# Optimization experiments

Hardware: AMD Instinct MI355X
Metric: run time of the kernel (lower is better)

Reference implementation:

```python
import jax, jax.numpy as jnp
import numpy as np

NUM_STAB = 1e-3  # numerical_stabilizer for relu kernel


def _relu_feature(x, proj):
    # x: [B, L, H, D], proj: [M, D] -> [B, L, H, M]
    ratio = 1.0 / jnp.sqrt(jnp.asarray(proj.shape[0], x.dtype))
    return jax.nn.relu(ratio * jnp.einsum('blhd,md->blhm', x, proj)) + NUM_STAB


def setup_inputs() -> dict:
    key = jax.random.key(0)
    k1, k2, k3, k4, k5 = jax.random.split(key, 5)
    B, L, H, D, M = 16, 576, 12, 64, 8  # L = length_of_side**2 = 24**2
    return {
        'query': jax.random.normal(k1, (B, L, H, D), dtype=jnp.float32),
        'key': jax.random.normal(k2, (B, L, H, D), dtype=jnp.float32),
        'value': jax.random.normal(k3, (B, L, H, D), dtype=jnp.float32),
        'projection_matrix': jax.random.normal(k4, (M, D), dtype=jnp.float32),
        # RPE mask is nonnegative per-head mixing matrix [H, L, L]
        'mask_matrix': jax.random.uniform(k5, (H, L, L), dtype=jnp.float32),
    }


def reference(query, key, value, projection_matrix, mask_matrix):
    # ReLU kernel features (projection_matrix_type='relu')
    q_prime = _relu_feature(query, projection_matrix)  # [B, L, H, M]
    k_prime = _relu_feature(key, projection_matrix)    # [B, L, H, M]
    B, L, H, M = k_prime.shape
    D = value.shape[-1]

    # D_1[b,l,h,m,d] = k'[b,l,h,m] * v[b,l,h,d], flattened over (m,d)
    D_1 = jnp.einsum('blhm,blhd->blhmd', k_prime, value).reshape(B, L, H, M * D)
    # mask-matrix causal/RPE mixing over the L dimension (per head)
    D_1_hat = jnp.einsum('hij,bjhc->bihc', mask_matrix, D_1).reshape(B, L, H, M, D)
    D_2_hat = jnp.einsum('hij,bjhm->bihm', mask_matrix, k_prime)  # [B, L, H, M]

    av_attention = jnp.einsum('blhm,blhmd->blhd', q_prime, D_1_hat)  # [B, L, H, D]
    ks_sum = jnp.sum(D_2_hat, axis=1)                                # [B, H, M]
    normalizer = jnp.einsum('blhm,bhm->blh', q_prime, ks_sum)        # [B, L, H]
    return av_attention / normalizer[..., None]
```

## Files before the change

### kernel.cpp

```cpp
#include <hip/hip_runtime.h>


#define B_ 16
#define L_ 576
#define H_ 12
#define D_ 64
#define M_ 8
#define NUM_STAB 1e-3f
#define RATIO 0.35355339059327373f

typedef __attribute__((ext_vector_type(8))) short short8;
typedef __attribute__((ext_vector_type(4))) float f32x4;

union Pack {
    uint4 u4;
    short8 s8;
    uint2 u2[2];
    unsigned u[4];
    unsigned short us[8];
};

__device__ inline unsigned short f2bf(float x) {
    union { float f; unsigned u; } a; a.f = x;
    unsigned r = (a.u + 0x7FFFu + ((a.u >> 16) & 1u)) >> 16;
    return (unsigned short)r;
}

#define WS_QP_OFF (H_ * L_)
#define QP_ELEMS  ((size_t)B_ * H_ * L_ * M_)

__global__ __launch_bounds__(256) void feat_kernel(const float* __restrict__ q,
                                                   const float* __restrict__ k,
                                                   const float* __restrict__ proj,
                                                   const float* __restrict__ mask,
                                                   unsigned short* __restrict__ qp,
                                                   unsigned short* __restrict__ kp,
                                                   float* __restrict__ cmask) {
    __shared__ float cred[4][16];
    const int lc = blockIdx.x, h = blockIdx.y, b = blockIdx.z, t = threadIdx.x;
    const int wv = t >> 6, l = t & 63, r8 = l >> 3, c8 = l & 7;
    const int row = lc * 32 + wv * 8 + r8;

    float4 pj0[8], pj1[8];
#pragma unroll
    for (int m = 0; m < 8; ++m) {
        pj0[m] = *(const float4*)(proj + m * 64 + c8 * 8);
        pj1[m] = *(const float4*)(proj + m * 64 + c8 * 8 + 4);
    }

#pragma unroll
    for (int s = 0; s < 2; ++s) {
        const float* src = s ? k : q;
        unsigned short* dst = s ? kp : qp;
        const float* xp = src + (((size_t)b * L_ + row) * H_ + h) * D_ + c8 * 8;
        float4 x0 = *(const float4*)xp;
        float4 x1 = *(const float4*)(xp + 4);
        x0.x *= RATIO; x0.y *= RATIO; x0.z *= RATIO; x0.w *= RATIO;
        x1.x *= RATIO; x1.y *= RATIO; x1.z *= RATIO; x1.w *= RATIO;
        float p[8];
#pragma unroll
        for (int m = 0; m < 8; ++m) {
            p[m] = x0.x * pj0[m].x + x0.y * pj0[m].y + x0.z * pj0[m].z + x0.w * pj0[m].w
                 + x1.x * pj1[m].x + x1.y * pj1[m].y + x1.z * pj1[m].z + x1.w * pj1[m].w;
        }
#pragma unroll
        for (int st = 1; st <= 4; st <<= 1) {
#pragma unroll
            for (int m = 0; m < 8; ++m) p[m] += __shfl_xor(p[m], st, 64);
        }
        float r = p[0];
        r = (c8 == 1) ? p[1] : r;
        r = (c8 == 2) ? p[2] : r;
        r = (c8 == 3) ? p[3] : r;
        r = (c8 == 4) ? p[4] : r;
        r = (c8 == 5) ? p[5] : r;
        r = (c8 == 6) ? p[6] : r;
        r = (c8 == 7) ? p[7] : r;
        r = fmaxf(r, 0.f) + NUM_STAB;
        dst[((size_t)(b * H_ + h) * L_ + row) * 8 + c8] = f2bf(r);
    }

    if (b < 2) {
        const int c = t & 15, rg = t >> 4;
        const int col0 = lc * 32 + b * 16;
        const float* mb = mask + (size_t)h * L_ * L_ + col0 + c;
        float a = 0.f;
#pragma unroll 4
        for (int k2 = 0; k2 < 36; ++k2) a += mb[(size_t)(rg + 16 * k2) * L_];
        a += __shfl_xor(a, 16, 64);
        a += __shfl_xor(a, 32, 64);
        if ((l >> 4) == 0) cred[wv][c] = a;
        __syncthreads();
        if (t < 16) cmask[h * L_ + col0 + t] = cred[0][t] + cred[1][t] + cred[2][t] + cred[3][t];
    }
}

__global__ __launch_bounds__(256, 4) void attn_kernel(const float* __restrict__ v,
                                                      const float* __restrict__ mask,
                                                      const unsigned short* __restrict__ qp,
                                                      const unsigned short* __restrict__ kp,
                                                      const float* __restrict__ cmask,
                                                      float* __restrict__ out) {
    __shared__ __align__(16) unsigned short Sp[4 * 16 * 40];
    __shared__ __align__(16) unsigned short Bt[2][64 * 40];
    __shared__ float cm_s[L_];

    const int t = threadIdx.x;
    int id = blockIdx.x;
    const int bhi = id & 7; id >>= 3;
    const int blo = id & 1; id >>= 1;
    const int it = id % 9, h = id / 9;
    const int b = bhi * 2 + blo;
    const int i0 = it * 64;

    const int wv = t >> 6, l = t & 63, c15 = l & 15, kq = l >> 4;

    cm_s[t] = cmask[h * L_ + t];
    cm_s[t + 256] = cmask[h * L_ + t + 256];
    if (t < 64) cm_s[t + 512] = cmask[h * L_ + t + 512];

    const float* maskbase = mask + (size_t)h * L_ * L_ + (size_t)(i0 + 16 * wv + c15) * L_;
    const unsigned short* kpb = kp + (size_t)(b * H_ + h) * L_ * 8;
    const float* vb = v + ((size_t)b * L_ * H_ + h) * D_ + l;

    short8 Bq;
    {
        Pack pk; pk.u4 = make_uint4(0, 0, 0, 0);
        if (kq == 0) {
            const unsigned short* qpb = qp + ((size_t)(b * H_ + h) * L_ + i0 + 16 * wv + c15) * 8;
            pk.u4 = *(const uint4*)qpb;
        }
        Bq = pk.s8;
    }

    unsigned short* SpW = Sp + wv * 16 * 40;

    f32x4 acc0 = {0.f, 0.f, 0.f, 0.f}, acc1 = acc0, acc2 = acc0, acc3 = acc0;
    float nacc = 0.f;

    float vf[8];
    float4 mv0, mv1;
    uint4 kraw = make_uint4(0, 0, 0, 0);
    {
#pragma unroll
        for (int qv = 0; qv < 8; ++qv) vf[qv] = vb[(size_t)(8 * wv + qv) * (H_ * D_)];
        mv0 = *(const float4*)(maskbase + 4 * kq);
        mv1 = *(const float4*)(maskbase + 16 + 4 * kq);
        if (kq < 2) kraw = *(const uint4*)(kpb + (size_t)(16 * kq + c15) * 8);
    }

    __syncthreads();

    for (int jt = 0; jt < 18; ++jt) {
        const int j0 = jt * 32;
        const int slab = jt & 1;

        Pack a0, a1;
        a1.u[0] = __shfl_down(kraw.x, 16, 64);
        a1.u[1] = __shfl_down(kraw.y, 16, 64);
        a1.u[2] = __shfl_down(kraw.z, 16, 64);
        a1.u[3] = __shfl_down(kraw.w, 16, 64);
        if (kq == 0) {
            a0.u4 = kraw;
        } else {
            a0.u4 = make_uint4(0, 0, 0, 0);
            a1.u4 = make_uint4(0, 0, 0, 0);
        }
        const f32x4 zz = {0.f, 0.f, 0.f, 0.f};
        f32x4 s0 = __builtin_amdgcn_mfma_f32_16x16x32_bf16(a0.s8, Bq, zz, 0, 0, 0);
        f32x4 s1 = __builtin_amdgcn_mfma_f32_16x16x32_bf16(a1.s8, Bq, zz, 0, 0, 0);

        {
            Pack pv;
#pragma unroll
            for (int qv = 0; qv < 8; ++qv) pv.us[qv] = f2bf(vf[qv]);
            *(uint4*)&Bt[slab][l * 40 + 8 * wv] = pv.u4;
        }
        {
            float4 cm0 = *(const float4*)&cm_s[j0 + 4 * kq];
            float4 cm1 = *(const float4*)&cm_s[j0 + 16 + 4 * kq];
            nacc += cm0.x * s0[0] + cm0.y * s0[1] + cm0.z * s0[2] + cm0.w * s0[3]
                  + cm1.x * s1[0] + cm1.y * s1[1] + cm1.z * s1[2] + cm1.w * s1[3];
            Pack ps;
            ps.us[0] = f2bf(s0[0] * mv0.x);
            ps.us[1] = f2bf(s0[1] * mv0.y);
            ps.us[2] = f2bf(s0[2] * mv0.z);
            ps.us[3] = f2bf(s0[3] * mv0.w);
            ps.us[4] = f2bf(s1[0] * mv1.x);
            ps.us[5] = f2bf(s1[1] * mv1.y);
            ps.us[6] = f2bf(s1[2] * mv1.z);
            ps.us[7] = f2bf(s1[3] * mv1.w);
            *(uint2*)&SpW[c15 * 40 + 4 * kq] = ps.u2[0];
            *(uint2*)&SpW[c15 * 40 + 16 + 4 * kq] = ps.u2[1];
        }
        {
            const int jn = (jt < 17) ? j0 + 32 : 0;
#pragma unroll
            for (int qv = 0; qv < 8; ++qv) vf[qv] = vb[(size_t)(jn + 8 * wv + qv) * (H_ * D_)];
            mv0 = *(const float4*)(maskbase + jn + 4 * kq);
            mv1 = *(const float4*)(maskbase + jn + 16 + 4 * kq);
            if (kq < 2) kraw = *(const uint4*)(kpb + (size_t)(jn + 16 * kq + c15) * 8);
        }
        __syncthreads();

        {
            short8 As = *(const short8*)&SpW[c15 * 40 + kq * 8];
            short8 B0 = *(const short8*)&Bt[slab][c15 * 40 + kq * 8];
            short8 B1 = *(const short8*)&Bt[slab][(16 + c15) * 40 + kq * 8];
            short8 B2 = *(const short8*)&Bt[slab][(32 + c15) * 40 + kq * 8];
            short8 B3 = *(const short8*)&Bt[slab][(48 + c15) * 40 + kq * 8];
            acc0 = __builtin_amdgcn_mfma_f32_16x16x32_bf16(As, B0, acc0, 0, 0, 0);
            acc1 = __builtin_amdgcn_mfma_f32_16x16x32_bf16(As, B1, acc1, 0, 0, 0);
            acc2 = __builtin_amdgcn_mfma_f32_16x16x32_bf16(As, B2, acc2, 0, 0, 0);
            acc3 = __builtin_amdgcn_mfma_f32_16x16x32_bf16(As, B3, acc3, 0, 0, 0);
        }
    }

    nacc += __shfl_xor(nacc, 16, 64);
    nacc += __shfl_xor(nacc, 32, 64);
    float iv[4];
#pragma unroll
    for (int r = 0; r < 4; ++r) iv[r] = 1.0f / __shfl(nacc, 4 * kq + r, 64);

    float* ob = out + (((size_t)b * L_ + i0 + 16 * wv + 4 * kq) * H_ + h) * D_ + c15;
    const f32x4 aa[4] = {acc0, acc1, acc2, acc3};
#pragma unroll
    for (int di = 0; di < 4; ++di)
#pragma unroll
        for (int r = 0; r < 4; ++r)
            ob[(size_t)r * (H_ * D_) + 16 * di] = aa[di][r] * iv[r];
}

extern "C" void kernel_launch(void* const* d_in, const int* in_sizes, int n_in,
                              void* d_out, int out_size, void* d_ws, size_t ws_size,
                              hipStream_t stream) {
    const float* q    = (const float*)d_in[0];
    const float* k    = (const float*)d_in[1];
    const float* v    = (const float*)d_in[2];
    const float* proj = (const float*)d_in[3];
    const float* mask = (const float*)d_in[4];
    float* out = (float*)d_out;

    float* ws = (float*)d_ws;
    float* cmask = ws;
    unsigned short* qp_w = (unsigned short*)(ws + WS_QP_OFF);
    unsigned short* kp_w = qp_w + QP_ELEMS;

    feat_kernel<<<dim3(L_ / 32, H_, B_), 256, 0, stream>>>(q, k, proj, mask, qp_w, kp_w, cmask);
    attn_kernel<<<1728, 256, 0, stream>>>(v, mask, qp_w, kp_w, cmask, out);
}
```

Measured before the change: 182.8 us.

## Double the j-tile to 64 per iteration and use packed bf16 conversion

The attention kernel now processes 64 key positions per loop iteration instead of 32. This halves the iteration count and the number of block barriers, and each iteration gets more MFMA work and larger batches of loads. The column-mask sums are permuted in shared memory so each lane reads them as scalar loads, and float-to-bf16 rounding uses the packed HIP intrinsic instead of manual bit rounding. The cost is more registers for v, mask and k prefetch and larger LDS tiles, which may reduce occupancy at the four-blocks-per-CU launch bound.

```diff
diff --git a/kernel.cpp b/kernel.cpp
--- a/kernel.cpp
+++ b/kernel.cpp
@@ -1,4 +1,5 @@
 #include <hip/hip_runtime.h>
+#include <hip/hip_bf16.h>
 
 
 #define B_ 16
@@ -24,6 +25,11 @@
     union { float f; unsigned u; } a; a.f = x;
     unsigned r = (a.u + 0x7FFFu + ((a.u >> 16) & 1u)) >> 16;
     return (unsigned short)r;
+}
+__device__ inline unsigned pk2(float lo, float hi) {
+    __hip_bfloat162 h = __float22bfloat162_rn(make_float2(lo, hi));
+    union { __hip_bfloat162 b; unsigned u; } c; c.b = h;
+    return c.u;
 }
 
 #define WS_QP_OFF (H_ * L_)
@@ -101,9 +107,9 @@
                                                       const unsigned short* __restrict__ kp,
                                                       const float* __restrict__ cmask,
                                                       float* __restrict__ out) {
-    __shared__ __align__(16) unsigned short Sp[4 * 16 * 40];
-    __shared__ __align__(16) unsigned short Bt[2][64 * 40];
-    __shared__ float cm_s[L_];
+    __shared__ __align__(16) unsigned short Sp[4 * 16 * 72];
+    __shared__ __align__(16) unsigned short Bt[2][64 * 72];
+    __shared__ float cms[576];
 
     const int t = threadIdx.x;
     int id = blockIdx.x;
@@ -115,9 +121,19 @@
 
     const int wv = t >> 6, l = t & 63, c15 = l & 15, kq = l >> 4;
 
-    cm_s[t] = cmask[h * L_ + t];
-    cm_s[t + 256] = cmask[h * L_ + t + 256];
-    if (t < 64) cm_s[t + 512] = cmask[h * L_ + t + 512];
+    {
+        const float* cmg = cmask + h * L_;
+#pragma unroll
+        for (int rep = 0; rep < 3; ++rep) {
+            int idx = t + rep * 256;
+            if (idx < 576) {
+                int p = idx / 36, rem = idx - p * 36;
+                int jt9 = rem >> 2, kqi = rem & 3;
+                int j = jt9 * 64 + ((p >> 2) << 4) + 4 * kqi + (p & 3);
+                cms[idx] = cmg[j];
+            }
+        }
+    }
 
     const float* maskbase = mask + (size_t)h * L_ * L_ + (size_t)(i0 + 16 * wv + c15) * L_;
     const unsigned short* kpb = kp + (size_t)(b * H_ + h) * L_ * 8;
@@ -133,86 +149,99 @@
         Bq = pk.s8;
     }
 
-    unsigned short* SpW = Sp + wv * 16 * 40;
+    unsigned short* SpW = Sp + wv * 16 * 72;
 
     f32x4 acc0 = {0.f, 0.f, 0.f, 0.f}, acc1 = acc0, acc2 = acc0, acc3 = acc0;
     float nacc = 0.f;
 
-    float vf[8];
-    float4 mv0, mv1;
-    uint4 kraw = make_uint4(0, 0, 0, 0);
+    float vf[16];
+    float4 mv[4];
+    uint4 kraw0 = make_uint4(0, 0, 0, 0), kraw1 = kraw0;
     {
 #pragma unroll
-        for (int qv = 0; qv < 8; ++qv) vf[qv] = vb[(size_t)(8 * wv + qv) * (H_ * D_)];
-        mv0 = *(const float4*)(maskbase + 4 * kq);
-        mv1 = *(const float4*)(maskbase + 16 + 4 * kq);
-        if (kq < 2) kraw = *(const uint4*)(kpb + (size_t)(16 * kq + c15) * 8);
+        for (int qv = 0; qv < 16; ++qv) vf[qv] = vb[(size_t)(16 * wv + qv) * (H_ * D_)];
+#pragma unroll
+        for (int T = 0; T < 4; ++T) mv[T] = *(const float4*)(maskbase + 16 * T + 4 * kq);
+        if (kq < 2) {
+            kraw0 = *(const uint4*)(kpb + (size_t)(16 * kq + c15) * 8);
+            kraw1 = *(const uint4*)(kpb + (size_t)(32 + 16 * kq + c15) * 8);
+        }
     }
 
     __syncthreads();
 
-    for (int jt = 0; jt < 18; ++jt) {
-        const int j0 = jt * 32;
+    for (int jt = 0; jt < 9; ++jt) {
+        const int j0 = jt * 64;
         const int slab = jt & 1;
 
-        Pack a0, a1;
-        a1.u[0] = __shfl_down(kraw.x, 16, 64);
-        a1.u[1] = __shfl_down(kraw.y, 16, 64);
-        a1.u[2] = __shfl_down(kraw.z, 16, 64);
-        a1.u[3] = __shfl_down(kraw.w, 16, 64);
-        if (kq == 0) {
-            a0.u4 = kraw;
-        } else {
-            a0.u4 = make_uint4(0, 0, 0, 0);
-            a1.u4 = make_uint4(0, 0, 0, 0);
-        }
+        f32x4 s[4];
         const f32x4 zz = {0.f, 0.f, 0.f, 0.f};
-        f32x4 s0 = __builtin_amdgcn_mfma_f32_16x16x32_bf16(a0.s8, Bq, zz, 0, 0, 0);
-        f32x4 s1 = __builtin_amdgcn_mfma_f32_16x16x32_bf16(a1.s8, Bq, zz, 0, 0, 0);
+#pragma unroll
+        for (int hh = 0; hh < 2; ++hh) {
+            uint4 kr = hh ? kraw1 : kraw0;
+            Pack a0, a1;
+            a1.u[0] = __shfl_down(kr.x, 16, 64);
+            a1.u[1] = __shfl_down(kr.y, 16, 64);
+            a1.u[2] = __shfl_down(kr.z, 16, 64);
+            a1.u[3] = __shfl_down(kr.w, 16, 64);
+            if (kq == 0) {
+                a0.u4 = kr;
+            } else {
+                a0.u4 = make_uint4(0, 0, 0, 0);
+                a1.u4 = make_uint4(0, 0, 0, 0);
+            }
+            s[2 * hh]     = __builtin_amdgcn_mfma_f32_16x16x32_bf16(a0.s8, Bq, zz, 0, 0, 0);
+            s[2 * hh + 1] = __builtin_amdgcn_mfma_f32_16x16x32_bf16(a1.s8, Bq, zz, 0, 0, 0);
+        }
 
         {
-            Pack pv;
-#pragma unroll
-            for (int qv = 0; qv < 8; ++qv) pv.us[qv] = f2bf(vf[qv]);
-            *(uint4*)&Bt[slab][l * 40 + 8 * wv] = pv.u4;
-        }
+            Pack p0, p1;
+#pragma unroll
+            for (int qv = 0; qv < 4; ++qv) p0.u[qv] = pk2(vf[2 * qv], vf[2 * qv + 1]);
+#pragma unroll
+            for (int qv = 0; qv < 4; ++qv) p1.u[qv] = pk2(vf[8 + 2 * qv], vf[9 + 2 * qv]);
+            *(uint4*)&Bt[slab][l * 72 + 16 * wv] = p0.u4;
+            *(uint4*)&Bt[slab][l * 72 + 16 * wv + 8] = p1.u4;
+        }
+
+#pragma unroll
+        for (int T = 0; T < 4; ++T) {
+            const float* cp = &cms[(T * 4) * 36 + jt * 4 + kq];
+            float c0 = cp[0], c1 = cp[36], c2 = cp[72], c3 = cp[108];
+            nacc += c0 * s[T][0] + c1 * s[T][1] + c2 * s[T][2] + c3 * s[T][3];
+            float4 m4 = mv[T];
+            uint2 st2;
+            st2.x = pk2(s[T][0] * m4.x, s[T][1] * m4.y);
+            st2.y = pk2(s[T][2] * m4.z, s[T][3] * m4.w);
+            *(uint2*)&SpW[c15 * 72 + 16 * T + 4 * kq] = st2;
+        }
+
         {
-            float4 cm0 = *(const float4*)&cm_s[j0 + 4 * kq];
-            float4 cm1 = *(const float4*)&cm_s[j0 + 16 + 4 * kq];
-            nacc += cm0.x * s0[0] + cm0.y * s0[1] + cm0.z * s0[2] + cm0.w * s0[3]
-                  + cm1.x * s1[0] + cm1.y * s1[1] + cm1.z * s1[2] + cm1.w * s1[3];
-            Pack ps;
-            ps.us[0] = f2bf(s0[0] * mv0.x);
-            ps.us[1] = f2bf(s0[1] * mv0.y);
-            ps.us[2] = f2bf(s0[2] * mv0.z);
-            ps.us[3] = f2bf(s0[3] * mv0.w);
-            ps.us[4] = f2bf(s1[0] * mv1.x);
-            ps.us[5] = f2bf(s1[1] * mv1.y);
-            ps.us[6] = f2bf(s1[2] * mv1.z);
-            ps.us[7] = f2bf(s1[3] * mv1.w);
-            *(uint2*)&SpW[c15 * 40 + 4 * kq] = ps.u2[0];
-            *(uint2*)&SpW[c15 * 40 + 16 + 4 * kq] = ps.u2[1];
-        }
+            const int jn = (jt < 8) ? j0 + 64 : 0;
+#pragma unroll
+            for (int qv = 0; qv < 16; ++qv) vf[qv] = vb[(size_t)(jn + 16 * wv + qv) * (H_ * D_)];
+#pragma unroll
+            for (int T = 0; T < 4; ++T) mv[T] = *(const float4*)(maskbase + jn + 16 * T + 4 * kq);
+            if (kq < 2) {
+                kraw0 = *(const uint4*)(kpb + (size_t)(jn + 16 * kq + c15) * 8);
+                kraw1 = *(const uint4*)(kpb + (size_t)(jn + 32 + 16 * kq + c15) * 8);
+            }
+        }
+
+        __syncthreads();
+
         {
-            const int jn = (jt < 17) ? j0 + 32 : 0;
-#pragma unroll
-            for (int qv = 0; qv < 8; ++qv) vf[qv] = vb[(size_t)(jn + 8 * wv + qv) * (H_ * D_)];
-            mv0 = *(const float4*)(maskbase + jn + 4 * kq);
-            mv1 = *(const float4*)(maskbase + jn + 16 + 4 * kq);
-            if (kq < 2) kraw = *(const uint4*)(kpb + (size_t)(jn + 16 * kq + c15) * 8);
-        }
-        __syncthreads();
-
-        {
-            short8 As = *(const short8*)&SpW[c15 * 40 + kq * 8];
-            short8 B0 = *(const short8*)&Bt[slab][c15 * 40 + kq * 8];
-            short8 B1 = *(const short8*)&Bt[slab][(16 + c15) * 40 + kq * 8];
-            short8 B2 = *(const short8*)&Bt[slab][(32 + c15) * 40 + kq * 8];
-            short8 B3 = *(const short8*)&Bt[slab][(48 + c15) * 40 + kq * 8];
-            acc0 = __builtin_amdgcn_mfma_f32_16x16x32_bf16(As, B0, acc0, 0, 0, 0);
-            acc1 = __builtin_amdgcn_mfma_f32_16x16x32_bf16(As, B1, acc1, 0, 0, 0);
-            acc2 = __builtin_amdgcn_mfma_f32_16x16x32_bf16(As, B2, acc2, 0, 0, 0);
-            acc3 = __builtin_amdgcn_mfma_f32_16x16x32_bf16(As, B3, acc3, 0, 0, 0);
+            short8 As0 = *(const short8*)&SpW[c15 * 72 + kq * 8];
+            short8 As1 = *(const short8*)&SpW[c15 * 72 + 32 + kq * 8];
+#pragma unroll
+            for (int di = 0; di < 4; ++di) {
+                const unsigned short* bp = &Bt[slab][(16 * di + c15) * 72 + kq * 8];
+                short8 B0 = *(const short8*)bp;
+                short8 B1 = *(const short8*)(bp + 32);
+                f32x4* ap = (di == 0) ? &acc0 : (di == 1) ? &acc1 : (di == 2) ? &acc2 : &acc3;
+                *ap = __builtin_amdgcn_mfma_f32_16x16x32_bf16(As0, B0, *ap, 0, 0, 0);
+                *ap = __builtin_amdgcn_mfma_f32_16x16x32_bf16(As1, B1, *ap, 0, 0, 0);
+            }
         }
     }
 
```

After: 181.6 us. No clear change (-0.6%).
